# Optimization experiments

Hardware: AMD Instinct MI355X
Metric: run time of the kernel (lower is better)

## Reference

```python
import jax, jax.numpy as jnp
import numpy as np

EPS = 1e-08

def setup_inputs() -> dict:
    key = jax.random.key(0)
    ten = jax.random.normal(key, (64, 3, 512, 512), dtype=jnp.float32)
    return {"ten": ten}

def reference(ten):
    # Instance-norm-like: per (n,c) mean and unbiased std over (H,W)
    x = ten.astype(jnp.float32)
    mn = jnp.mean(x, axis=(2, 3), keepdims=True)
    hw = x.shape[2] * x.shape[3]
    var = jnp.sum((x - mn) ** 2, axis=(2, 3), keepdims=True) / (hw - 1)  # unbiased (ddof=1)
    std = jnp.sqrt(var) + EPS
    return (x - mn) / std
```

## Files before the change

kernel.cpp:

```cpp
#include <hip/hip_runtime.h>

#define HW_ELEMS (512 * 512)
#define HW4      (HW_ELEMS / 4)
#define NC 192
#define BPC 8
#define EPS 1e-8f

typedef float fx4 __attribute__((ext_vector_type(4)));

__global__ __launch_bounds__(256) void instnorm_partial(
    const float* __restrict__ in, float2* __restrict__ partials)
{
    const int c = blockIdx.x >> 3;
    const int b = blockIdx.x & (BPC - 1);
    const fx4* p = reinterpret_cast<const fx4*>(in)
                 + (size_t)c * HW4 + (size_t)b * (HW4 / BPC);
    const int t = threadIdx.x;

    float sum = 0.f, sumsq = 0.f;
#pragma unroll
    for (int k = 0; k < HW4 / BPC / 256; ++k) {
        fx4 v = p[t + k * 256];
        sum   += (v.x + v.y) + (v.z + v.w);
        sumsq += (v.x * v.x + v.y * v.y) + (v.z * v.z + v.w * v.w);
    }

#pragma unroll
    for (int off = 32; off > 0; off >>= 1) {
        sum   += __shfl_down(sum, off, 64);
        sumsq += __shfl_down(sumsq, off, 64);
    }

    __shared__ float s_sum[4];
    __shared__ float s_sq[4];
    const int wave = t >> 6;
    if ((t & 63) == 0) { s_sum[wave] = sum; s_sq[wave] = sumsq; }
    __syncthreads();

    if (t == 0) {
        float S = s_sum[0] + s_sum[1] + s_sum[2] + s_sum[3];
        float Q = s_sq[0] + s_sq[1] + s_sq[2] + s_sq[3];
        partials[blockIdx.x] = make_float2(S, Q);
    }
}

__global__ __launch_bounds__(256) void instnorm_apply(
    const float* __restrict__ in, float* __restrict__ out,
    const float2* __restrict__ partials)
{
    const int c = blockIdx.x >> 8;
    float S = 0.f, Q = 0.f;
#pragma unroll
    for (int b = 0; b < BPC; ++b) {
        float2 pq = partials[c * BPC + b];
        S += pq.x; Q += pq.y;
    }
    const float n = (float)HW_ELEMS;
    float mean = S / n;
    float var  = (Q - S * S / n) / (n - 1.0f);
    if (var < 0.f) var = 0.f;
    float rstd = 1.0f / (sqrtf(var) + EPS);

    const size_t i4 = (size_t)blockIdx.x * 256 + threadIdx.x;
    fx4 v = reinterpret_cast<const fx4*>(in)[i4];
    fx4 r;
    r.x = (v.x - mean) * rstd;
    r.y = (v.y - mean) * rstd;
    r.z = (v.z - mean) * rstd;
    r.w = (v.w - mean) * rstd;
    __builtin_nontemporal_store(r, reinterpret_cast<fx4*>(out) + i4);
}

extern "C" void kernel_launch(void* const* d_in, const int* in_sizes, int n_in,
                              void* d_out, int out_size, void* d_ws, size_t ws_size,
                              hipStream_t stream) {
    const float* in = (const float*)d_in[0];
    float* out = (float*)d_out;
    float2* partials = (float2*)d_ws;

    instnorm_partial<<<NC * BPC, 256, 0, stream>>>(in, partials);

    const size_t total4 = (size_t)NC * HW4;
    instnorm_apply<<<(int)(total4 / 256), 256, 0, stream>>>(in, out, partials);
}
```

Measured before the change: 91.08 us.

## Fuse reduction and normalization into cooperative kernel with per-channel semaphores

Replaces the two-pass partial-sum plus apply kernels with a single cooperative kernel where each block reduces its slice, publishes partials, spins on a per-channel counter until all slices for that channel are done, then normalizes its own slice. The intent is to re-read the slice while it is likely still cache-resident and avoid a second launch. It adds a memset launch, spin-waiting, and a fallback path (with reversed block order) if the cooperative launch fails.

```diff
diff --git a/kernel.cpp b/kernel.cpp
--- a/kernel.cpp
+++ b/kernel.cpp
@@ -3,57 +3,59 @@
 #define HW_ELEMS (512 * 512)
 #define HW4      (HW_ELEMS / 4)
 #define NC 192
+#define THREADS 256
 #define BPC 8
+#define SLICE4 (HW4 / BPC)
+#define NBLK (NC * BPC)
 #define EPS 1e-8f
 
 typedef float fx4 __attribute__((ext_vector_type(4)));
 
-__global__ __launch_bounds__(256) void instnorm_partial(
-    const float* __restrict__ in, float2* __restrict__ partials)
+__global__ __launch_bounds__(THREADS, 6) void instnorm_coop(
+    const float* __restrict__ in, float* __restrict__ out,
+    float* __restrict__ psum, float* __restrict__ psq,
+    unsigned* __restrict__ sem)
 {
-    const int c = blockIdx.x >> 3;
-    const int b = blockIdx.x & (BPC - 1);
-    const fx4* p = reinterpret_cast<const fx4*>(in)
-                 + (size_t)c * HW4 + (size_t)b * (HW4 / BPC);
+    const int s = blockIdx.x;
+    const int c = s >> 3;
+    const int b = s & (BPC - 1);
+    const size_t base = (size_t)c * HW4 + (size_t)b * SLICE4;
+    const fx4* p = reinterpret_cast<const fx4*>(in) + base;
     const int t = threadIdx.x;
 
-    float sum = 0.f, sumsq = 0.f;
-#pragma unroll
-    for (int k = 0; k < HW4 / BPC / 256; ++k) {
-        fx4 v = p[t + k * 256];
-        sum   += (v.x + v.y) + (v.z + v.w);
-        sumsq += (v.x * v.x + v.y * v.y) + (v.z * v.z + v.w * v.w);
+    float sum = 0.f, sq = 0.f;
+#pragma unroll 4
+    for (int k = 0; k < SLICE4 / THREADS; ++k) {
+        fx4 v = p[t + k * THREADS];
+        sum += (v.x + v.y) + (v.z + v.w);
+        sq  += v.x * v.x + v.y * v.y + v.z * v.z + v.w * v.w;
     }
-
 #pragma unroll
     for (int off = 32; off > 0; off >>= 1) {
-        sum   += __shfl_down(sum, off, 64);
-        sumsq += __shfl_down(sumsq, off, 64);
+        sum += __shfl_down(sum, off, 64);
+        sq  += __shfl_down(sq,  off, 64);
     }
-
     __shared__ float s_sum[4];
     __shared__ float s_sq[4];
-    const int wave = t >> 6;
-    if ((t & 63) == 0) { s_sum[wave] = sum; s_sq[wave] = sumsq; }
+    if ((t & 63) == 0) { s_sum[t >> 6] = sum; s_sq[t >> 6] = sq; }
     __syncthreads();
 
     if (t == 0) {
         float S = s_sum[0] + s_sum[1] + s_sum[2] + s_sum[3];
-        float Q = s_sq[0] + s_sq[1] + s_sq[2] + s_sq[3];
-        partials[blockIdx.x] = make_float2(S, Q);
+        float Q = s_sq[0]  + s_sq[1]  + s_sq[2]  + s_sq[3];
+        __hip_atomic_store(&psum[s], S, __ATOMIC_RELAXED, __HIP_MEMORY_SCOPE_AGENT);
+        __hip_atomic_store(&psq[s],  Q, __ATOMIC_RELAXED, __HIP_MEMORY_SCOPE_AGENT);
+        __hip_atomic_fetch_add(&sem[c], 1u, __ATOMIC_RELEASE, __HIP_MEMORY_SCOPE_AGENT);
+        while (__hip_atomic_load(&sem[c], __ATOMIC_ACQUIRE, __HIP_MEMORY_SCOPE_AGENT) < BPC)
+            __builtin_amdgcn_s_sleep(1);
     }
-}
+    __syncthreads();
 
-__global__ __launch_bounds__(256) void instnorm_apply(
-    const float* __restrict__ in, float* __restrict__ out,
-    const float2* __restrict__ partials)
-{
-    const int c = blockIdx.x >> 8;
     float S = 0.f, Q = 0.f;
 #pragma unroll
-    for (int b = 0; b < BPC; ++b) {
-        float2 pq = partials[c * BPC + b];
-        S += pq.x; Q += pq.y;
+    for (int i = 0; i < BPC; ++i) {
+        S += __hip_atomic_load(&psum[c * BPC + i], __ATOMIC_RELAXED, __HIP_MEMORY_SCOPE_AGENT);
+        Q += __hip_atomic_load(&psq[c * BPC + i],  __ATOMIC_RELAXED, __HIP_MEMORY_SCOPE_AGENT);
     }
     const float n = (float)HW_ELEMS;
     float mean = S / n;
@@ -61,7 +63,66 @@
     if (var < 0.f) var = 0.f;
     float rstd = 1.0f / (sqrtf(var) + EPS);
 
-    const size_t i4 = (size_t)blockIdx.x * 256 + threadIdx.x;
+#pragma unroll 4
+    for (int k = 0; k < SLICE4 / THREADS; ++k) {
+        fx4 v = p[t + k * THREADS];
+        fx4 r;
+        r.x = (v.x - mean) * rstd;
+        r.y = (v.y - mean) * rstd;
+        r.z = (v.z - mean) * rstd;
+        r.w = (v.w - mean) * rstd;
+        __builtin_nontemporal_store(
+            r, reinterpret_cast<fx4*>(out) + base + t + k * THREADS);
+    }
+}
+
+__global__ __launch_bounds__(256) void instnorm_partial(
+    const float* __restrict__ in, float* __restrict__ psum, float* __restrict__ psq)
+{
+    const int c = blockIdx.x >> 3;
+    const int b = blockIdx.x & (BPC - 1);
+    const fx4* p = reinterpret_cast<const fx4*>(in)
+                 + (size_t)c * HW4 + (size_t)b * SLICE4;
+    const int t = threadIdx.x;
+    float sum = 0.f, sq = 0.f;
+#pragma unroll 4
+    for (int k = 0; k < SLICE4 / 256; ++k) {
+        fx4 v = p[t + k * 256];
+        sum += (v.x + v.y) + (v.z + v.w);
+        sq  += v.x * v.x + v.y * v.y + v.z * v.z + v.w * v.w;
+    }
+#pragma unroll
+    for (int off = 32; off > 0; off >>= 1) {
+        sum += __shfl_down(sum, off, 64);
+        sq  += __shfl_down(sq,  off, 64);
+    }
+    __shared__ float s_sum[4];
+    __shared__ float s_sq[4];
+    if ((t & 63) == 0) { s_sum[t >> 6] = sum; s_sq[t >> 6] = sq; }
+    __syncthreads();
+    if (t == 0) {
+        psum[blockIdx.x] = s_sum[0] + s_sum[1] + s_sum[2] + s_sum[3];
+        psq[blockIdx.x]  = s_sq[0] + s_sq[1] + s_sq[2] + s_sq[3];
+    }
+}
+
+__global__ __launch_bounds__(256) void instnorm_apply_rev(
+    const float* __restrict__ in, float* __restrict__ out,
+    const float* __restrict__ psum, const float* __restrict__ psq)
+{
+    const int nblk = (int)((size_t)NC * HW4 / 256);
+    const int rb = nblk - 1 - blockIdx.x;
+    const int c = rb >> 8;
+    float S = 0.f, Q = 0.f;
+#pragma unroll
+    for (int i = 0; i < BPC; ++i) { S += psum[c * BPC + i]; Q += psq[c * BPC + i]; }
+    const float n = (float)HW_ELEMS;
+    float mean = S / n;
+    float var  = (Q - S * S / n) / (n - 1.0f);
+    if (var < 0.f) var = 0.f;
+    float rstd = 1.0f / (sqrtf(var) + EPS);
+
+    const size_t i4 = (size_t)rb * 256 + threadIdx.x;
     fx4 v = reinterpret_cast<const fx4*>(in)[i4];
     fx4 r;
     r.x = (v.x - mean) * rstd;
@@ -76,10 +137,19 @@
                               hipStream_t stream) {
     const float* in = (const float*)d_in[0];
     float* out = (float*)d_out;
-    float2* partials = (float2*)d_ws;
+    float*    psum = (float*)d_ws;
+    float*    psq  = psum + NBLK;
+    unsigned* sem  = (unsigned*)(psq + NBLK);
 
-    instnorm_partial<<<NC * BPC, 256, 0, stream>>>(in, partials);
+    hipMemsetAsync(sem, 0, NC * sizeof(unsigned), stream);
 
-    const size_t total4 = (size_t)NC * HW4;
-    instnorm_apply<<<(int)(total4 / 256), 256, 0, stream>>>(in, out, partials);
+    void* args[] = { (void*)&in, (void*)&out, (void*)&psum, (void*)&psq, (void*)&sem };
+    hipError_t rc = hipLaunchCooperativeKernel((const void*)instnorm_coop,
+                                               dim3(NBLK), dim3(THREADS),
+                                               args, 0, stream);
+    if (rc != hipSuccess) {
+        instnorm_partial<<<NBLK, 256, 0, stream>>>(in, psum, psq);
+        const size_t total4 = (size_t)NC * HW4;
+        instnorm_apply_rev<<<(int)(total4 / 256), 256, 0, stream>>>(in, out, psum, psq);
+    }
 }
```

Result: slower. 194.1 us (+113.1%).

## Split stats and apply passes into channel chunks for cache reuse

Applied to the files above, without the earlier changes.

Processes the 192 channels in three chunks, launching the stats kernel and then the apply kernel for each chunk. The 64-channel working set (64 MB) may then stay resident in the large last-level cache between the stats read and the apply read, instead of the full 192 MB being streamed twice from HBM. In exchange it issues six launches instead of two, and the stats kernel for each chunk only has 512 blocks, which can underfill the GPU. The partials are also split into separate sum and sumsq arrays.

```diff
diff --git a/kernel.cpp b/kernel.cpp
--- a/kernel.cpp
+++ b/kernel.cpp
@@ -3,65 +3,60 @@
 #define HW_ELEMS (512 * 512)
 #define HW4      (HW_ELEMS / 4)
 #define NC 192
+#define NCHUNK 3
+#define CPC (NC / NCHUNK)
 #define BPC 8
 #define EPS 1e-8f
 
 typedef float fx4 __attribute__((ext_vector_type(4)));
 
 __global__ __launch_bounds__(256) void instnorm_partial(
-    const float* __restrict__ in, float2* __restrict__ partials)
+    const float* __restrict__ in, float* __restrict__ psum,
+    float* __restrict__ psq, int ch0)
 {
-    const int c = blockIdx.x >> 3;
+    const int c = ch0 + (blockIdx.x >> 3);
     const int b = blockIdx.x & (BPC - 1);
     const fx4* p = reinterpret_cast<const fx4*>(in)
                  + (size_t)c * HW4 + (size_t)b * (HW4 / BPC);
     const int t = threadIdx.x;
 
-    float sum = 0.f, sumsq = 0.f;
+    float sum = 0.f, sq = 0.f;
 #pragma unroll
     for (int k = 0; k < HW4 / BPC / 256; ++k) {
         fx4 v = p[t + k * 256];
-        sum   += (v.x + v.y) + (v.z + v.w);
-        sumsq += (v.x * v.x + v.y * v.y) + (v.z * v.z + v.w * v.w);
+        sum += (v.x + v.y) + (v.z + v.w);
+        sq  += v.x * v.x + v.y * v.y + v.z * v.z + v.w * v.w;
     }
-
 #pragma unroll
     for (int off = 32; off > 0; off >>= 1) {
-        sum   += __shfl_down(sum, off, 64);
-        sumsq += __shfl_down(sumsq, off, 64);
+        sum += __shfl_down(sum, off, 64);
+        sq  += __shfl_down(sq,  off, 64);
     }
-
-    __shared__ float s_sum[4];
-    __shared__ float s_sq[4];
-    const int wave = t >> 6;
-    if ((t & 63) == 0) { s_sum[wave] = sum; s_sq[wave] = sumsq; }
+    __shared__ float s_red[8];
+    if ((t & 63) == 0) { s_red[t >> 6] = sum; s_red[4 + (t >> 6)] = sq; }
     __syncthreads();
-
     if (t == 0) {
-        float S = s_sum[0] + s_sum[1] + s_sum[2] + s_sum[3];
-        float Q = s_sq[0] + s_sq[1] + s_sq[2] + s_sq[3];
-        partials[blockIdx.x] = make_float2(S, Q);
+        const int s = c * BPC + b;
+        psum[s] = s_red[0] + s_red[1] + s_red[2] + s_red[3];
+        psq[s]  = s_red[4] + s_red[5] + s_red[6] + s_red[7];
     }
 }
 
 __global__ __launch_bounds__(256) void instnorm_apply(
     const float* __restrict__ in, float* __restrict__ out,
-    const float2* __restrict__ partials)
+    const float* __restrict__ psum, const float* __restrict__ psq, int ch0)
 {
-    const int c = blockIdx.x >> 8;
+    const size_t i4 = (size_t)ch0 * HW4 + (size_t)blockIdx.x * 256 + threadIdx.x;
+    const int c = (int)(i4 >> 16);
     float S = 0.f, Q = 0.f;
 #pragma unroll
-    for (int b = 0; b < BPC; ++b) {
-        float2 pq = partials[c * BPC + b];
-        S += pq.x; Q += pq.y;
-    }
+    for (int i = 0; i < BPC; ++i) { S += psum[c * BPC + i]; Q += psq[c * BPC + i]; }
     const float n = (float)HW_ELEMS;
     float mean = S / n;
     float var  = (Q - S * S / n) / (n - 1.0f);
     if (var < 0.f) var = 0.f;
     float rstd = 1.0f / (sqrtf(var) + EPS);
 
-    const size_t i4 = (size_t)blockIdx.x * 256 + threadIdx.x;
     fx4 v = reinterpret_cast<const fx4*>(in)[i4];
     fx4 r;
     r.x = (v.x - mean) * rstd;
@@ -76,10 +71,14 @@
                               hipStream_t stream) {
     const float* in = (const float*)d_in[0];
     float* out = (float*)d_out;
-    float2* partials = (float2*)d_ws;
+    float* psum = (float*)d_ws;
+    float* psq  = psum + NC * BPC;
 
-    instnorm_partial<<<NC * BPC, 256, 0, stream>>>(in, partials);
+    const int statsBlk = CPC * BPC;
+    const int applyBlk = CPC * (HW4 / 256);
 
-    const size_t total4 = (size_t)NC * HW4;
-    instnorm_apply<<<(int)(total4 / 256), 256, 0, stream>>>(in, out, partials);
+    for (int ch0 = 0; ch0 < NC; ch0 += CPC) {
+        instnorm_partial<<<statsBlk, 256, 0, stream>>>(in, psum, psq, ch0);
+        instnorm_apply<<<applyBlk, 256, 0, stream>>>(in, out, psum, psq, ch0);
+    }
 }
```

Result: slower. 96.96 us (+6.5%).
